# Optimization experiments

Hardware: AMD Instinct MI355X
Metric: run time of the kernel (lower is better)

The kernel has to match this reference:

```python
import jax, jax.numpy as jnp
import numpy as np

N_HEAD = 16
ROPE_BASE = 10000.0


def _rope(x, cos, sin):
    # x: [B,H,T,D]; cos/sin: [T,D/2] broadcast over B,H
    half = x.shape[-1] // 2
    x1, x2 = x[..., :half], x[..., half:]
    return jnp.concatenate([x1 * cos - x2 * sin, x1 * sin + x2 * cos], axis=-1)


def setup_inputs() -> dict:
    key = jax.random.key(0)
    k1, k2, k3 = jax.random.split(key, 3)
    C = 2048
    x = jax.random.normal(k1, (4, 2048, C), dtype=jnp.float32)
    w_qkv = jax.random.normal(k2, (C, 3 * C), dtype=jnp.float32) * 0.02
    w_proj = jax.random.normal(k3, (C, C), dtype=jnp.float32) * 0.02
    return {"x": x, "w_qkv": w_qkv, "w_proj": w_proj}


def reference(x, w_qkv, w_proj):
    B, T, C = x.shape
    H = N_HEAD
    D = C // H
    half = D // 2

    qkv = x @ w_qkv  # [B,T,3C]
    q, k, v = jnp.split(qkv, 3, axis=-1)
    # [B,T,C] -> [B,H,T,D]
    q = q.reshape(B, T, H, D).transpose(0, 2, 1, 3)
    k = k.reshape(B, T, H, D).transpose(0, 2, 1, 3)
    v = v.reshape(B, T, H, D).transpose(0, 2, 1, 3)

    # RoPE cache (start_pos = 0, no kv_cache / prefill path)
    inv_freq = 1.0 / (ROPE_BASE ** (jnp.arange(half, dtype=jnp.float32) / half))
    pos = jnp.arange(T, dtype=jnp.float32)
    freqs = pos[:, None] * inv_freq[None, :]  # [T, half]
    cos, sin = jnp.cos(freqs), jnp.sin(freqs)

    q = _rope(q, cos, sin)
    k = _rope(k, cos, sin)

    # scaled dot-product attention with explicit causal mask
    att = jnp.einsum("bhqd,bhkd->bhqk", q, k) / jnp.sqrt(jnp.asarray(D, x.dtype))
    causal = jnp.arange(T)[:, None] >= jnp.arange(T)[None, :]  # [T,T] bool
    att = jnp.where(causal, att, jnp.asarray(-jnp.inf, att.dtype))
    att = jax.nn.softmax(att, axis=-1)
    # dropout = identity (eval mode)
    out = jnp.einsum("bhqk,bhkd->bhqd", att, v)
    out = out.transpose(0, 2, 1, 3).reshape(B, T, C)
    out = out @ w_proj
    return out, k, v  # (output, new kv-cache)
```

## Files before the change

### kernel.cpp

```cpp
#include <hip/hip_runtime.h>
#include <math.h>

#define CDIM 2048
#define TDIM 2048
#define BDIM 4
#define HDIM 16
#define DDIM 128
#define M1   (BDIM * TDIM)
#define N1   (3 * CDIM)
#define KK   CDIM
#define NT   32

typedef unsigned short u16;
typedef __bf16 bf16x8 __attribute__((ext_vector_type(8)));
typedef float f32x4 __attribute__((ext_vector_type(4)));

__device__ __forceinline__ u16 f2b(float f) {
  union { float f; unsigned u; } x; x.f = f;
  unsigned r = x.u + 0x7fffu + ((x.u >> 16) & 1u);
  return (u16)(r >> 16);
}

__device__ __forceinline__ void gload_lds16(const void* g, void* l) {
  __builtin_amdgcn_global_load_lds(
      (__attribute__((address_space(1))) void*)g,
      (__attribute__((address_space(3))) void*)l, 16, 0, 0);
}

__global__ void prep(const float* __restrict__ x, u16* __restrict__ xb,
                     const float* __restrict__ w_qkv, u16* __restrict__ wqkvT,
                     const float* __restrict__ w_proj, u16* __restrict__ wprojT,
                     float* __restrict__ cosT, float* __restrict__ sinT) {
  __shared__ float tile[32][33];
  const int gb = blockIdx.x;
  if (gb < 16384) {
    int i = gb * 256 + threadIdx.x;
    float4 v = ((const float4*)x)[i];
    unsigned long long o = (unsigned long long)f2b(v.x)
                         | ((unsigned long long)f2b(v.y) << 16)
                         | ((unsigned long long)f2b(v.z) << 32)
                         | ((unsigned long long)f2b(v.w) << 48);
    ((unsigned long long*)xb)[i] = o;
  } else if (gb < 32768) {
    const float* w; u16* wt; int N, r;
    if (gb < 28672) { w = w_qkv;  wt = wqkvT;  N = N1;   r = gb - 16384; }
    else            { w = w_proj; wt = wprojT; N = CDIM; r = gb - 28672; }
    const int nblk = N >> 5;
    const int n0 = (r % nblk) * 32, k0 = (r / nblk) * 32;
    const int tx = threadIdx.x & 31, ty = threadIdx.x >> 5;
    for (int rr = ty; rr < 32; rr += 8)
      tile[rr][tx] = w[(k0 + rr) * N + n0 + tx];
    __syncthreads();
    for (int rr = ty; rr < 32; rr += 8)
      wt[(n0 + rr) * KK + k0 + tx] = f2b(tile[tx][rr]);
  } else {
    int i = (gb - 32768) * 256 + threadIdx.x;
    int t = i >> 6, d = i & 63;
    float inv = exp2f(-(float)d * (13.287712379549449f / 64.0f));
    float a = (float)t * inv;
    cosT[i] = cosf(a);
    sinT[i] = sinf(a);
  }
}


#define VMW4 asm volatile("s_waitcnt vmcnt(4)" ::: "memory");
#define VMW2 asm volatile("s_waitcnt vmcnt(2)" ::: "memory");
#define VMW0 asm volatile("s_waitcnt vmcnt(0)" ::: "memory");
#define NOWAIT

#define GEMM256_TILE(bufA_, bufB_, nA_, nB_, kno_, STG, WMID, WEND)            \
  {                                                                            \
    __builtin_amdgcn_s_barrier();        \
    bf16x8 aX[4][2], aY[4][2], bX[2][2], bY[2][2];                             \
                                                     \
    _Pragma("unroll")                                                          \
    for (int i = 0; i < 4; ++i)                                                \
      _Pragma("unroll")                                                        \
      for (int kh = 0; kh < 2; ++kh)                                           \
        aX[i][kh] = *(const bf16x8*)&(bufA_)[aoff + i * 1024 +                 \
                                             (((kh * 4 + quad) ^ rsw) * 8)];   \
    _Pragma("unroll")                                                          \
    for (int j = 0; j < 2; ++j)                                                \
      _Pragma("unroll")                                                        \
      for (int kh = 0; kh < 2; ++kh)                                           \
        bX[j][kh] = *(const bf16x8*)&(bufB_)[boff + j * 1024 +                 \
                                             (((kh * 4 + quad) ^ rsw) * 8)];   \
                                                          \
    __builtin_amdgcn_s_setprio(1);                                             \
    _Pragma("unroll")                                                          \
    for (int i = 0; i < 4; ++i)                                                \
      _Pragma("unroll")                                                        \
      for (int j = 0; j < 2; ++j)                                              \
        _Pragma("unroll")                                                      \
        for (int kh = 0; kh < 2; ++kh)                                         \
          acc[i][j] = __builtin_amdgcn_mfma_f32_16x16x32_bf16(                 \
              aX[i][kh], bX[j][kh], acc[i][j], 0, 0, 0);                       \
    __builtin_amdgcn_s_setprio(0);                                             \
                                                  \
    _Pragma("unroll")                                                          \
    for (int j = 0; j < 2; ++j)                                                \
      _Pragma("unroll")                                                        \
      for (int kh = 0; kh < 2; ++kh)                                           \
        bY[j][kh] = *(const bf16x8*)&(bufB_)[8192 + boff + j * 1024 +          \
                                             (((kh * 4 + quad) ^ rsw) * 8)];   \
    if (STG) {                                                                 \
      _Pragma("unroll")                                                        \
      for (int q = 0; q < 2; ++q)                                              \
        gload_lds16(AgBase + (q * 128) * KK + (kno_), &(nA_)[q * 4096 + ldsw]);\
      _Pragma("unroll")                                                        \
      for (int q = 0; q < 2; ++q)                                              \
        gload_lds16(BgBase + (q * 128) * KK + (kno_),                          \
                    &(nB_)[q * 4096 + ldsw]);                                  \
    }                                                                          \
    WMID                                                                       \
    __builtin_amdgcn_s_barrier();                       \
                                                          \
    __builtin_amdgcn_s_setprio(1);                                             \
    _Pragma("unroll")                                                          \
    for (int i = 0; i < 4; ++i)                                                \
      _Pragma("unroll")                                                        \
      for (int j = 0; j < 2; ++j)                                              \
        _Pragma("unroll")                                                      \
        for (int kh = 0; kh < 2; ++kh)                                         \
          acc[i][2 + j] = __builtin_amdgcn_mfma_f32_16x16x32_bf16(             \
              aX[i][kh], bY[j][kh], acc[i][2 + j], 0, 0, 0);                   \
    __builtin_amdgcn_s_setprio(0);                                             \
                                                  \
    _Pragma("unroll")                                                          \
    for (int i = 0; i < 4; ++i)                                                \
      _Pragma("unroll")                                                        \
      for (int kh = 0; kh < 2; ++kh)                                           \
        aY[i][kh] = *(const bf16x8*)&(bufA_)[8192 + aoff + i * 1024 +          \
                                             (((kh * 4 + quad) ^ rsw) * 8)];   \
    if (STG) {                                                                 \
      _Pragma("unroll")                                                        \
      for (int q = 0; q < 2; ++q)                                              \
        gload_lds16(BgBase + (q * 128 + 32) * KK + (kno_),                     \
                    &(nB_)[8192 + q * 4096 + ldsw]);                           \
    }                                                                          \
                                                          \
    __builtin_amdgcn_s_setprio(1);                                             \
    _Pragma("unroll")                                                          \
    for (int i = 0; i < 4; ++i)                                                \
      _Pragma("unroll")                                                        \
      for (int j = 0; j < 2; ++j)                                              \
        _Pragma("unroll")                                                      \
        for (int kh = 0; kh < 2; ++kh)                                         \
          acc[4 + i][2 + j] = __builtin_amdgcn_mfma_f32_16x16x32_bf16(         \
              aY[i][kh], bY[j][kh], acc[4 + i][2 + j], 0, 0, 0);               \
    __builtin_amdgcn_s_setprio(0);                                             \
    if (STG) {                                                                 \
      _Pragma("unroll")                                                        \
      for (int q = 0; q < 2; ++q)                                              \
        gload_lds16(AgBase + (q * 128 + 64) * KK + (kno_),                     \
                    &(nA_)[8192 + q * 4096 + ldsw]);                           \
    }                                                                          \
                                                          \
    __builtin_amdgcn_s_setprio(1);                                             \
    _Pragma("unroll")                                                          \
    for (int i = 0; i < 4; ++i)                                                \
      _Pragma("unroll")                                                        \
      for (int j = 0; j < 2; ++j)                                              \
        _Pragma("unroll")                                                      \
        for (int kh = 0; kh < 2; ++kh)                                         \
          acc[4 + i][j] = __builtin_amdgcn_mfma_f32_16x16x32_bf16(             \
              aY[i][kh], bX[j][kh], acc[4 + i][j], 0, 0, 0);                   \
    __builtin_amdgcn_s_setprio(0);                                             \
    WEND                                                                       \
  }

#define GEMM256_MAINLOOP(APTR, BPTR)                                           \
  const int rA = lane >> 3, cA = lane & 7;                                     \
  const int w8r = wave * 8 + rA;                                               \
  const int swz8 = (cA ^ rA) * 8;                                              \
  const u16* AgBase = (APTR) + (m0 + w8r) * KK + swz8;                         \
  const int nb = ((w8r >> 5) * 64) + (w8r & 31);                               \
  const u16* BgBase = (BPTR) + (n0 + nb) * KK + swz8;                          \
  const int ldsw = wave * 512;                                                 \
  const int rsw = c16 & 7;                                                     \
  const int aoff = (((wave >> 2) * 64) + c16) * 64;                            \
  const int boff = (((wave & 3) * 32) + c16) * 64;                             \
  f32x4 acc[8][4];                                                             \
  {                                                                            \
    f32x4 z = {0.f, 0.f, 0.f, 0.f};                                            \
    _Pragma("unroll")                                                          \
    for (int i = 0; i < 8; ++i)                                                \
      _Pragma("unroll")                                                        \
      for (int j = 0; j < 4; ++j) acc[i][j] = z;                               \
  }                                                                            \
  _Pragma("unroll")                                                            \
  for (int q = 0; q < 2; ++q)                                                  \
    gload_lds16(AgBase + (q * 128) * KK, &lds[q * 4096 + ldsw]);               \
  _Pragma("unroll")                                                            \
  for (int q = 0; q < 2; ++q)                                                  \
    gload_lds16(BgBase + (q * 128) * KK, &lds[32768 + q * 4096 + ldsw]);       \
  _Pragma("unroll")                                                            \
  for (int q = 0; q < 2; ++q)                                                  \
    gload_lds16(BgBase + (q * 128 + 32) * KK,                                  \
                &lds[32768 + 8192 + q * 4096 + ldsw]);                         \
  _Pragma("unroll")                                                            \
  for (int q = 0; q < 2; ++q)                                                  \
    gload_lds16(AgBase + (q * 128 + 64) * KK, &lds[8192 + q * 4096 + ldsw]);   \
  VMW2                                                                         \
  for (int kt = 0; kt < NT - 1; ++kt) {                                        \
    const int cur = kt & 1;                                                    \
    const u16* bA = &lds[cur * 16384];                                         \
    const u16* bB = &lds[32768 + cur * 16384];                                 \
    u16* nA = &lds[(cur ^ 1) * 16384];                                         \
    u16* nB = &lds[32768 + (cur ^ 1) * 16384];                                 \
    const int kno = (kt + 1) * 64;                                             \
    GEMM256_TILE(bA, bB, nA, nB, kno, 1, VMW4, VMW2)                           \
  }                                                                            \
  GEMM256_TILE((&lds[16384]), (&lds[32768 + 16384]), (&lds[0]),                \
               (&lds[32768]), 0, 0, VMW0, NOWAIT)

__global__ __launch_bounds__(512, 1) void gemm_qkv(
    const u16* __restrict__ A,
    const u16* __restrict__ Bt,
    const float* __restrict__ cosT, const float* __restrict__ sinT,
    u16* __restrict__ qb, u16* __restrict__ kb,
    float* __restrict__ kout, float* __restrict__ vout,
    u16* __restrict__ vtout)
{
  extern __shared__ __align__(16) u16 lds[];
  const int tid = threadIdx.x, wave = tid >> 6, lane = tid & 63;
  const int quad = lane >> 4, c16 = lane & 15;
  const int bid = blockIdx.y * 24 + blockIdx.x;
  const int swz = (bid & 7) * 96 + (bid >> 3);
  const int m0 = (swz / 24) * 256, n0 = (swz % 24) * 256;

  GEMM256_MAINLOOP(A, Bt)

  float* cbuf = (float*)lds;
  const int mat = n0 >> 11;
  const int hbase = (n0 & 2047) >> 7;
  const float qscale = 0.1275178689414753f;
#pragma unroll
  for (int pass = 0; pass < 4; ++pass) {
    __syncthreads();
    if ((wave >> 2) == (pass >> 1)) {
#pragma unroll
      for (int i = 0; i < 4; ++i) {
        const int mf = (pass & 1) * 4 + i;
#pragma unroll
        for (int j = 0; j < 4; ++j)
#pragma unroll
          for (int r = 0; r < 4; ++r)
            cbuf[(i * 16 + quad * 4 + r) * 261 + (wave & 3) * 64 + j * 16 + c16] = acc[mf][j][r];
      }
    }
    __syncthreads();
#pragma unroll
    for (int it = 0; it < 16; ++it) {
      int p = it * 512 + tid;
      int lr = p >> 7;
      int hc = (p >> 6) & 1;
      int d = p & 63;
      float x1 = cbuf[lr * 261 + hc * 128 + d];
      float x2 = cbuf[lr * 261 + hc * 128 + 64 + d];
      int mg = m0 + pass * 64 + lr;
      int b = mg >> 11, t = mg & 2047;
      int h = hbase + hc;
      int idx = ((b * HDIM + h) * TDIM + t) * DDIM + d;
      if (mat == 2) {
        vout[idx] = x1; vout[idx + 64] = x2;
      } else {
        float cs = cosT[t * 64 + d], sn = sinT[t * 64 + d];
        float o1 = x1 * cs - x2 * sn;
        float o2 = x1 * sn + x2 * cs;
        if (mat == 0) {
          qb[idx] = f2b(o1 * qscale); qb[idx + 64] = f2b(o2 * qscale);
        } else {
          kout[idx] = o1; kout[idx + 64] = o2;
          kb[idx] = f2b(o1); kb[idx + 64] = f2b(o2);
        }
      }
    }
    if (mat == 2) {
#pragma unroll
      for (int it = 0; it < 16; ++it) {
        int p = it * 512 + tid;
        int tl = p & 63;
        int c2 = p >> 6;
        float xA = cbuf[tl * 261 + c2];
        float xB = cbuf[tl * 261 + 128 + c2];
        int mg = m0 + pass * 64 + tl;
        int b = mg >> 11, t = mg & 2047;
        vtout[((b * HDIM + hbase) * DDIM + c2) * TDIM + t] = f2b(xA);
        vtout[((b * HDIM + hbase + 1) * DDIM + c2) * TDIM + t] = f2b(xB);
      }
    }
  }
}

__global__ __launch_bounds__(512, 1) void gemm_proj(
    const u16* __restrict__ A,
    const u16* __restrict__ Bt,
    float* __restrict__ out)
{
  extern __shared__ __align__(16) u16 lds[];
  const int tid = threadIdx.x, wave = tid >> 6, lane = tid & 63;
  const int quad = lane >> 4, c16 = lane & 15;
  const int bid = blockIdx.y * 8 + blockIdx.x;
  const int swz = (bid & 7) * 32 + (bid >> 3);
  const int m0 = (swz >> 3) * 256, n0 = (swz & 7) * 256;

  GEMM256_MAINLOOP(A, Bt)

  const int wm = (wave >> 2) * 128, wn = (wave & 3) * 64;
#pragma unroll
  for (int mf = 0; mf < 8; ++mf)
#pragma unroll
    for (int nf = 0; nf < 4; ++nf)
#pragma unroll
      for (int r = 0; r < 4; ++r)
        out[(m0 + wm + mf * 16 + quad * 4 + r) * CDIM + n0 + wn + nf * 16 + c16] =
            acc[mf][nf][r];
}

__global__ __launch_bounds__(512, 4) void attn(
    const u16* __restrict__ qb, const u16* __restrict__ kb,
    const u16* __restrict__ vt, u16* __restrict__ att)
{
  extern __shared__ __align__(16) u16 sh[];
  u16* const psm = sh + 32768;

  const int tid = threadIdx.x, wave = tid >> 6, lane = tid & 63;
  const int quad = lane >> 4, c16 = lane & 15;
  const int bx = blockIdx.x;
  const int bh = blockIdx.y;

  const int rlK = wave * 4 + (lane >> 4), chK = lane & 15;
  const int rlV = wave * 8 + (lane >> 3), chV = lane & 7;

  for (int hv = 0; hv < 2; ++hv) {
    const int qt = hv ? (7 - bx) : (bx + 8);
    const int q0 = qt * 128;

    {
      const u16* qg = qb + (bh * TDIM + q0) * DDIM;
#pragma unroll
      for (int r = 0; r < 4; ++r) {
        int row = r * 32 + rlK;
        gload_lds16(qg + row * DDIM + (chK ^ (row & 15)) * 8,
                    &sh[(r * 32 + wave * 4) * 128]);
      }
    }
    __syncthreads();
    bf16x8 qf[4];
#pragma unroll
    for (int kp = 0; kp < 4; ++kp)
      qf[kp] = *(const bf16x8*)&sh[(wave * 16 + c16) * 128 +
                                   (((kp * 4 + quad) ^ c16) * 8)];
    __syncthreads();

    f32x4 o[8];
    f32x4 zero = {0.f, 0.f, 0.f, 0.f};
#pragma unroll
    for (int jd = 0; jd < 8; ++jd) o[jd] = zero;
    float lrow[4];
#pragma unroll
    for (int r = 0; r < 4; ++r) lrow[r] = 0.f;

    const int nchunk = 2 * qt + 2;
    const int lastrow = q0 + wave * 16 + 15;

#define STAGE_KV(kcs, bufbase)                                                 \
    {                                                                          \
      const int kcs0 = (kcs) * 64;                                             \
      const u16* kg = kb + (bh * TDIM + kcs0) * DDIM;                          \
      _Pragma("unroll")                                                        \
      for (int r = 0; r < 2; ++r) {                                            \
        int row = r * 32 + rlK;                                                \
        gload_lds16(kg + row * DDIM + (chK ^ (row & 15)) * 8,                  \
                    &sh[(bufbase) + (r * 32 + wave * 4) * 128]);               \
      }                                                                        \
      const u16* vg = vt + bh * (DDIM * TDIM) + kcs0;                          \
      _Pragma("unroll")                                                        \
      for (int r = 0; r < 2; ++r) {                                            \
        int row = r * 64 + rlV;                                                \
        gload_lds16(vg + row * TDIM + (chV ^ (row & 7)) * 8,                   \
                    &sh[(bufbase) + 8192 + (r * 64 + wave * 8) * 64]);         \
      }                                                                        \
    }

    STAGE_KV(0, 0)

    for (int kc = 0; kc < nchunk; ++kc) {
      const int kc0 = kc * 64;
      const int cur = kc & 1;
      const u16* ksm = sh + cur * 16384;
      const u16* vsm = ksm + 8192;

      if (kc + 1 < nchunk) {
        STAGE_KV(kc + 1, (cur ^ 1) * 16384)
        asm volatile("s_waitcnt vmcnt(4)" ::: "memory");
      } else {
        asm volatile("s_waitcnt vmcnt(0)" ::: "memory");
      }
      asm volatile("s_barrier" ::: "memory");

      if (kc0 <= lastrow) {
        f32x4 st[4];
#pragma unroll
        for (int j = 0; j < 4; ++j) st[j] = zero;
#pragma unroll
        for (int kp = 0; kp < 4; ++kp) {
#pragma unroll
          for (int j = 0; j < 4; ++j) {
            bf16x8 bk = *(const bf16x8*)&ksm[(j * 16 + c16) * 128 +
                                             (((kp * 4 + quad) ^ c16) * 8)];
            st[j] = __builtin_amdgcn_mfma_f32_16x16x32_bf16(qf[kp], bk, st[j], 0, 0, 0);
          }
        }

        u16* const pw = psm + wave * 1024;
        const bool dg = (kc0 + 63 > q0 + wave * 16);
        const int qrow_base = q0 + wave * 16 + quad * 4;
#pragma unroll
        for (int r = 0; r < 4; ++r) {
          const int row16 = quad * 4 + r;
          float sum = 0.f;
#pragma unroll
          for (int j = 0; j < 4; ++j) {
            float sv = st[j][r];
            if (dg && (kc0 + j * 16 + c16 > qrow_base + r)) sv = -INFINITY;
            float p = exp2f(sv - 8.0f);
            sum += p;
            int chunk = (j * 2 + (c16 >> 3)) ^ (row16 & 7);
            pw[row16 * 64 + chunk * 8 + (c16 & 7)] = f2b(p);
          }
          lrow[r] += sum;
        }

        asm volatile("s_waitcnt lgkmcnt(0)" ::: "memory");

#pragma unroll
        for (int s = 0; s < 2; ++s) {
          const int chp = ((s * 4 + quad) ^ (c16 & 7)) * 8;
          bf16x8 ap = *(const bf16x8*)&pw[c16 * 64 + chp];
#pragma unroll
          for (int jd = 0; jd < 8; ++jd) {
            bf16x8 bv = *(const bf16x8*)&vsm[(jd * 16 + c16) * 64 + chp];
            o[jd] = __builtin_amdgcn_mfma_f32_16x16x32_bf16(ap, bv, o[jd], 0, 0, 0);
          }
        }
      }
      asm volatile("s_barrier" ::: "memory");
    }
#undef STAGE_KV

    const int b = bh >> 4, h = bh & 15;
    float ri[4];
#pragma unroll
    for (int r = 0; r < 4; ++r) {
      float s = lrow[r];
      s += __shfl_xor(s, 1, 64);
      s += __shfl_xor(s, 2, 64);
      s += __shfl_xor(s, 4, 64);
      s += __shfl_xor(s, 8, 64);
      ri[r] = 1.f / s;
    }
#pragma unroll
    for (int jd = 0; jd < 8; ++jd)
#pragma unroll
      for (int r = 0; r < 4; ++r) {
        int t = q0 + wave * 16 + quad * 4 + r;
        att[(b * TDIM + t) * CDIM + h * DDIM + jd * 16 + c16] = f2b(o[jd][r] * ri[r]);
      }
    __syncthreads();
  }
}

extern "C" void kernel_launch(void* const* d_in, const int* in_sizes, int n_in,
                              void* d_out, int out_size, void* d_ws, size_t ws_size,
                              hipStream_t stream) {
  (void)in_sizes; (void)n_in; (void)out_size; (void)ws_size;
  const float* x      = (const float*)d_in[0];
  const float* w_qkv  = (const float*)d_in[1];
  const float* w_proj = (const float*)d_in[2];
  float* out  = (float*)d_out;
  float* kout = out + 16777216;
  float* vout = out + 2 * 16777216;

  char* ws = (char*)d_ws;
  u16*   xb     = (u16*)(ws);
  u16*   wqkvT  = (u16*)(ws + 33554432);
  u16*   wprojT = (u16*)(ws + 58720256);
  float* cosT   = (float*)(ws + 67108864);
  float* sinT   = (float*)(ws + 67633152);
  u16*   qb     = (u16*)(ws + 68157440);
  u16*   kb     = (u16*)(ws + 101711872);
  u16*   vt     = (u16*)(ws + 135266304);
  u16*   att    = xb;

  static int attr_set = 0;
  if (!attr_set) {
    hipFuncSetAttribute((const void*)gemm_qkv,
                        hipFuncAttributeMaxDynamicSharedMemorySize, 131072);
    hipFuncSetAttribute((const void*)gemm_proj,
                        hipFuncAttributeMaxDynamicSharedMemorySize, 131072);
    hipFuncSetAttribute((const void*)attn,
                        hipFuncAttributeMaxDynamicSharedMemorySize, 81920);
    attr_set = 1;
  }

  prep<<<33280, 256, 0, stream>>>(x, xb, w_qkv, wqkvT, w_proj, wprojT, cosT, sinT);
  gemm_qkv<<<dim3(24, 32), 512, 131072, stream>>>(xb, wqkvT, cosT, sinT, qb, kb, kout, vout, vt);
  attn<<<dim3(8, 64), 512, 81920, stream>>>(qb, kb, vt, att);
  gemm_proj<<<dim3(8, 32), 512, 131072, stream>>>(att, wprojT, out);
}
```

Measured before the change: 673.2 us.

## Process both paired causal query tiles concurrently in one 1024-thread attention block

```diff
diff --git a/kernel.cpp b/kernel.cpp
--- a/kernel.cpp
+++ b/kernel.cpp
@@ -319,7 +319,7 @@
             acc[mf][nf][r];
 }
 
-__global__ __launch_bounds__(512, 4) void attn(
+__global__ __launch_bounds__(1024, 4) void attn(
     const u16* __restrict__ qb, const u16* __restrict__ kb,
     const u16* __restrict__ vt, u16* __restrict__ att)
 {
@@ -331,146 +331,137 @@
   const int bx = blockIdx.x;
   const int bh = blockIdx.y;
 
-  const int rlK = wave * 4 + (lane >> 4), chK = lane & 15;
-  const int rlV = wave * 8 + (lane >> 3), chV = lane & 7;
-
-  for (int hv = 0; hv < 2; ++hv) {
-    const int qt = hv ? (7 - bx) : (bx + 8);
-    const int q0 = qt * 128;
-
-    {
-      const u16* qg = qb + (bh * TDIM + q0) * DDIM;
-#pragma unroll
-      for (int r = 0; r < 4; ++r) {
-        int row = r * 32 + rlK;
-        gload_lds16(qg + row * DDIM + (chK ^ (row & 15)) * 8,
-                    &sh[(r * 32 + wave * 4) * 128]);
-      }
-    }
-    __syncthreads();
-    bf16x8 qf[4];
-#pragma unroll
-    for (int kp = 0; kp < 4; ++kp)
-      qf[kp] = *(const bf16x8*)&sh[(wave * 16 + c16) * 128 +
-                                   (((kp * 4 + quad) ^ c16) * 8)];
-    __syncthreads();
-
-    f32x4 o[8];
-    f32x4 zero = {0.f, 0.f, 0.f, 0.f};
-#pragma unroll
-    for (int jd = 0; jd < 8; ++jd) o[jd] = zero;
-    float lrow[4];
-#pragma unroll
-    for (int r = 0; r < 4; ++r) lrow[r] = 0.f;
-
-    const int nchunk = 2 * qt + 2;
-    const int lastrow = q0 + wave * 16 + 15;
+  const int qtA = bx + 8, qtB = 7 - bx;
+  const int q0 = ((wave < 8) ? qtA : qtB) * 128;
+  const int rowbase = q0 + (wave & 7) * 16;
+
+  {
+    const int rl = lane >> 4, ch = lane & 15;
+#pragma unroll
+    for (int r = 0; r < 4; ++r) {
+      int lrow = r * 64 + wave * 4 + rl;
+      int trow = lrow & 127;
+      int gq0 = ((lrow >> 7) ? qtB : qtA) * 128;
+      gload_lds16(qb + (bh * TDIM + gq0 + trow) * DDIM + ((ch ^ (trow & 15)) * 8),
+                  &sh[(r * 64 + wave * 4) * 128]);
+    }
+  }
+  __syncthreads();
+  bf16x8 qf[4];
+#pragma unroll
+  for (int kp = 0; kp < 4; ++kp)
+    qf[kp] = *(const bf16x8*)&sh[(wave * 16 + c16) * 128 +
+                                 (((kp * 4 + quad) ^ c16) * 8)];
+  __syncthreads();
+
+  f32x4 o[8];
+  f32x4 zero = {0.f, 0.f, 0.f, 0.f};
+#pragma unroll
+  for (int jd = 0; jd < 8; ++jd) o[jd] = zero;
+  float lrow[4];
+#pragma unroll
+  for (int r = 0; r < 4; ++r) lrow[r] = 0.f;
+
+  const int nchunk = 2 * qtA + 2;
+  const int lastrow = rowbase + 15;
+
+  const int rK = wave * 4 + (lane >> 4), cK = lane & 15;
+  const int rV = wave * 8 + (lane >> 3), cV = lane & 7;
 
 #define STAGE_KV(kcs, bufbase)                                                 \
-    {                                                                          \
-      const int kcs0 = (kcs) * 64;                                             \
-      const u16* kg = kb + (bh * TDIM + kcs0) * DDIM;                          \
-      _Pragma("unroll")                                                        \
-      for (int r = 0; r < 2; ++r) {                                            \
-        int row = r * 32 + rlK;                                                \
-        gload_lds16(kg + row * DDIM + (chK ^ (row & 15)) * 8,                  \
-                    &sh[(bufbase) + (r * 32 + wave * 4) * 128]);               \
-      }                                                                        \
-      const u16* vg = vt + bh * (DDIM * TDIM) + kcs0;                          \
-      _Pragma("unroll")                                                        \
-      for (int r = 0; r < 2; ++r) {                                            \
-        int row = r * 64 + rlV;                                                \
-        gload_lds16(vg + row * TDIM + (chV ^ (row & 7)) * 8,                   \
-                    &sh[(bufbase) + 8192 + (r * 64 + wave * 8) * 64]);         \
-      }                                                                        \
-    }
-
-    STAGE_KV(0, 0)
-
-    for (int kc = 0; kc < nchunk; ++kc) {
-      const int kc0 = kc * 64;
-      const int cur = kc & 1;
-      const u16* ksm = sh + cur * 16384;
-      const u16* vsm = ksm + 8192;
-
-      if (kc + 1 < nchunk) {
-        STAGE_KV(kc + 1, (cur ^ 1) * 16384)
-        asm volatile("s_waitcnt vmcnt(4)" ::: "memory");
-      } else {
-        asm volatile("s_waitcnt vmcnt(0)" ::: "memory");
-      }
-      asm volatile("s_barrier" ::: "memory");
-
-      if (kc0 <= lastrow) {
-        f32x4 st[4];
-#pragma unroll
-        for (int j = 0; j < 4; ++j) st[j] = zero;
-#pragma unroll
-        for (int kp = 0; kp < 4; ++kp) {
-#pragma unroll
-          for (int j = 0; j < 4; ++j) {
-            bf16x8 bk = *(const bf16x8*)&ksm[(j * 16 + c16) * 128 +
-                                             (((kp * 4 + quad) ^ c16) * 8)];
-            st[j] = __builtin_amdgcn_mfma_f32_16x16x32_bf16(qf[kp], bk, st[j], 0, 0, 0);
-          }
-        }
-
-        u16* const pw = psm + wave * 1024;
-        const bool dg = (kc0 + 63 > q0 + wave * 16);
-        const int qrow_base = q0 + wave * 16 + quad * 4;
-#pragma unroll
-        for (int r = 0; r < 4; ++r) {
-          const int row16 = quad * 4 + r;
-          float sum = 0.f;
-#pragma unroll
-          for (int j = 0; j < 4; ++j) {
-            float sv = st[j][r];
-            if (dg && (kc0 + j * 16 + c16 > qrow_base + r)) sv = -INFINITY;
-            float p = exp2f(sv - 8.0f);
-            sum += p;
-            int chunk = (j * 2 + (c16 >> 3)) ^ (row16 & 7);
-            pw[row16 * 64 + chunk * 8 + (c16 & 7)] = f2b(p);
-          }
-          lrow[r] += sum;
-        }
-
-        asm volatile("s_waitcnt lgkmcnt(0)" ::: "memory");
-
-#pragma unroll
-        for (int s = 0; s < 2; ++s) {
-          const int chp = ((s * 4 + quad) ^ (c16 & 7)) * 8;
-          bf16x8 ap = *(const bf16x8*)&pw[c16 * 64 + chp];
-#pragma unroll
-          for (int jd = 0; jd < 8; ++jd) {
-            bf16x8 bv = *(const bf16x8*)&vsm[(jd * 16 + c16) * 64 + chp];
-            o[jd] = __builtin_amdgcn_mfma_f32_16x16x32_bf16(ap, bv, o[jd], 0, 0, 0);
-          }
+  {                                                                            \
+    const int kcs0 = (kcs) * 64;                                               \
+    gload_lds16(kb + (bh * TDIM + kcs0 + rK) * DDIM + ((cK ^ (rK & 15)) * 8),  \
+                &sh[(bufbase) + (wave * 4) * 128]);                            \
+    gload_lds16(vt + bh * (DDIM * TDIM) + rV * TDIM + kcs0 +                   \
+                    ((cV ^ (rV & 7)) * 8),                                     \
+                &sh[(bufbase) + 8192 + (wave * 8) * 64]);                      \
+  }
+
+  STAGE_KV(0, 0)
+
+  for (int kc = 0; kc < nchunk; ++kc) {
+    const int kc0 = kc * 64;
+    const int cur = kc & 1;
+    const u16* ksm = sh + cur * 16384;
+    const u16* vsm = ksm + 8192;
+
+    if (kc + 1 < nchunk) {
+      STAGE_KV(kc + 1, (cur ^ 1) * 16384)
+      asm volatile("s_waitcnt vmcnt(2)" ::: "memory");
+    } else {
+      asm volatile("s_waitcnt vmcnt(0)" ::: "memory");
+    }
+    asm volatile("s_barrier" ::: "memory");
+
+    if (kc0 <= lastrow) {
+      f32x4 st[4];
+#pragma unroll
+      for (int j = 0; j < 4; ++j) st[j] = zero;
+#pragma unroll
+      for (int kp = 0; kp < 4; ++kp) {
+#pragma unroll
+        for (int j = 0; j < 4; ++j) {
+          bf16x8 bk = *(const bf16x8*)&ksm[(j * 16 + c16) * 128 +
+                                           (((kp * 4 + quad) ^ c16) * 8)];
+          st[j] = __builtin_amdgcn_mfma_f32_16x16x32_bf16(qf[kp], bk, st[j], 0, 0, 0);
         }
       }
-      asm volatile("s_barrier" ::: "memory");
-    }
+
+      u16* const pw = psm + wave * 1024;
+      const bool dg = (kc0 + 63 > rowbase);
+      const int qrow_base = rowbase + quad * 4;
+#pragma unroll
+      for (int r = 0; r < 4; ++r) {
+        const int row16 = quad * 4 + r;
+        float sum = 0.f;
+#pragma unroll
+        for (int j = 0; j < 4; ++j) {
+          float sv = st[j][r];
+          if (dg && (kc0 + j * 16 + c16 > qrow_base + r)) sv = -INFINITY;
+          float p = exp2f(sv - 8.0f);
+          sum += p;
+          int chunk = (j * 2 + (c16 >> 3)) ^ (row16 & 7);
+          pw[row16 * 64 + chunk * 8 + (c16 & 7)] = f2b(p);
+        }
+        lrow[r] += sum;
+      }
+
+      asm volatile("s_waitcnt lgkmcnt(0)" ::: "memory");
+
+#pragma unroll
+      for (int s = 0; s < 2; ++s) {
+        const int chp = ((s * 4 + quad) ^ (c16 & 7)) * 8;
+        bf16x8 ap = *(const bf16x8*)&pw[c16 * 64 + chp];
+#pragma unroll
+        for (int jd = 0; jd < 8; ++jd) {
+          bf16x8 bv = *(const bf16x8*)&vsm[(jd * 16 + c16) * 64 + chp];
+          o[jd] = __builtin_amdgcn_mfma_f32_16x16x32_bf16(ap, bv, o[jd], 0, 0, 0);
+        }
+      }
+    }
+    asm volatile("s_barrier" ::: "memory");
+  }
 #undef STAGE_KV
 
-    const int b = bh >> 4, h = bh & 15;
-    float ri[4];
+  const int b = bh >> 4, h = bh & 15;
+  float ri[4];
+#pragma unroll
+  for (int r = 0; r < 4; ++r) {
+    float s = lrow[r];
+    s += __shfl_xor(s, 1, 64);
+    s += __shfl_xor(s, 2, 64);
+    s += __shfl_xor(s, 4, 64);
+    s += __shfl_xor(s, 8, 64);
+    ri[r] = 1.f / s;
+  }
+#pragma unroll
+  for (int jd = 0; jd < 8; ++jd)
 #pragma unroll
     for (int r = 0; r < 4; ++r) {
-      float s = lrow[r];
-      s += __shfl_xor(s, 1, 64);
-      s += __shfl_xor(s, 2, 64);
-      s += __shfl_xor(s, 4, 64);
-      s += __shfl_xor(s, 8, 64);
-      ri[r] = 1.f / s;
-    }
-#pragma unroll
-    for (int jd = 0; jd < 8; ++jd)
-#pragma unroll
-      for (int r = 0; r < 4; ++r) {
-        int t = q0 + wave * 16 + quad * 4 + r;
-        att[(b * TDIM + t) * CDIM + h * DDIM + jd * 16 + c16] = f2b(o[jd][r] * ri[r]);
-      }
-    __syncthreads();
-  }
+      int t = rowbase + quad * 4 + r;
+      att[(b * TDIM + t) * CDIM + h * DDIM + jd * 16 + c16] = f2b(o[jd][r] * ri[r]);
+    }
 }
 
 extern "C" void kernel_launch(void* const* d_in, const int* in_sizes, int n_in,
@@ -502,12 +493,12 @@
     hipFuncSetAttribute((const void*)gemm_proj,
                         hipFuncAttributeMaxDynamicSharedMemorySize, 131072);
     hipFuncSetAttribute((const void*)attn,
-                        hipFuncAttributeMaxDynamicSharedMemorySize, 81920);
+                        hipFuncAttributeMaxDynamicSharedMemorySize, 98304);
     attr_set = 1;
   }
 
   prep<<<33280, 256, 0, stream>>>(x, xb, w_qkv, wqkvT, w_proj, wprojT, cosT, sinT);
   gemm_qkv<<<dim3(24, 32), 512, 131072, stream>>>(xb, wqkvT, cosT, sinT, qb, kb, kout, vout, vt);
-  attn<<<dim3(8, 64), 512, 81920, stream>>>(qb, kb, vt, att);
+  attn<<<dim3(8, 64), 1024, 98304, stream>>>(qb, kb, vt, att);
   gemm_proj<<<dim3(8, 32), 512, 131072, stream>>>(att, wprojT, out);
 }
```

After: 701.1 us. 4.1% more time.
